# Kernel tuning notes

Hardware: AMD Instinct MI355X
Metric: run time of the kernel (lower is better)

## Reference

```python
import jax, jax.numpy as jnp
import numpy as np

N, F_IN, H, D = 4096, 512, 4, 64  # nodes, in_features, num_heads, head_dim (out_features = H*D = 256)
NEG_BIG = -9e15


def setup_inputs() -> dict:
    key = jax.random.key(0)
    k_x, k_adj, k_W, k_a = jax.random.split(key, 4)
    x = jax.random.normal(k_x, (N, F_IN), dtype=jnp.float32)
    adj = jax.random.randint(k_adj, (N, N), 0, 2, dtype=jnp.int32)
    # xavier_uniform-like scales
    W = jax.random.normal(k_W, (H, F_IN, D), dtype=jnp.float32) * np.float32((6.0 / (F_IN + D)) ** 0.5)
    a = jax.random.normal(k_a, (H, 2 * D), dtype=jnp.float32) * np.float32(0.1)
    bias = jnp.zeros((H * D,), dtype=jnp.float32)
    return {"x": x, "adj": adj, "W": W, "a": a, "bias": bias}


def reference(x, adj, W, a, bias):
    # Wx per head: [H, N, D]
    Wx = jnp.einsum('nf,hfd->hnd', x, W)
    # e[h,i,j] = leaky_relu(a[h,:D].Wx[h,i] + a[h,D:].Wx[h,j]) -- same math as concat form
    s_src = jnp.einsum('hnd,hd->hn', Wx, a[:, :D])  # [H, N]
    s_dst = jnp.einsum('hnd,hd->hn', Wx, a[:, D:])  # [H, N]
    e = jax.nn.leaky_relu(s_src[:, :, None] + s_dst[:, None, :], negative_slope=0.2)  # [H, N, N]
    masked = jnp.where(adj[None, :, :] > 0, e, jnp.float32(NEG_BIG))
    att = jax.nn.softmax(masked, axis=-1)  # row-wise softmax, [H, N, N]
    h = jnp.einsum('hij,hjd->hid', att, Wx)  # [H, N, D]
    out = h.transpose(1, 0, 2).reshape(x.shape[0], -1) + bias  # [N, H*D]
    return jax.nn.relu(out)
```

## Files before the change

### kernel.cpp

```cpp
#include <hip/hip_runtime.h>
#include <hip/hip_bf16.h>

#define NN   4096
#define FIN  512
#define NH   4
#define DD   64

typedef float f32x4 __attribute__((ext_vector_type(4)));
typedef short s16x8 __attribute__((ext_vector_type(8)));

__device__ __forceinline__ void gld_lds16(const void* g, void* l) {
  __builtin_amdgcn_global_load_lds(
      (const __attribute__((address_space(1))) void*)g,
      (__attribute__((address_space(3))) void*)l, 16, 0, 0);
}

__device__ __forceinline__ short bfbits(float f) {
  union { float f; unsigned u; } v; v.f = f;
  unsigned r = v.u + 0x7FFFu + ((v.u >> 16) & 1u);
  return (short)(r >> 16);
}

__device__ __forceinline__ int pkbf(float a, float b) {
  union { float f; unsigned u; } va, vb;
  va.f = a; vb.f = b;
  unsigned ra = (va.u + 0x7FFFu + ((va.u >> 16) & 1u)) >> 16;
  unsigned rb = (vb.u + 0x7FFFu + ((vb.u >> 16) & 1u)) & 0xFFFF0000u;
  return (int)(ra | rb);
}

__device__ __forceinline__ float hexp2(float x) {
#if __has_builtin(__builtin_amdgcn_exp2f)
  return __builtin_amdgcn_exp2f(x);
#else
  return __builtin_exp2f(x);
#endif
}

__global__ __launch_bounds__(512) void gat_k1(
    const float* __restrict__ x, const float* __restrict__ W,
    const float* __restrict__ a,
    short* __restrict__ WxT, float* __restrict__ ssrc, float* __restrict__ sdst)
{
  __shared__ __align__(16) char sm[34816];
  short* As = (short*)sm;
  short* Bs = (short*)(sm + 17408);
  float* Cs = (float*)sm;

  const int bx = blockIdx.x;
  const int h  = bx >> 6;
  const int r  = bx & 63;
  const int n0 = r * 64;
  const int t  = threadIdx.x;
  const int w  = t >> 6, lane = t & 63;
  const int lm = lane & 15, q = lane >> 4;
  const int rs = w & 3, cs = w >> 2;

  f32x4 acc[2] = {};
  const float* Wh = W + (size_t)h * (FIN * DD);

  for (int kq = 0; kq < 4; ++kq) {
    {
      const int row = t >> 3, fl = (t & 7) * 16;
      const float* xp = x + (size_t)(n0 + row) * FIN + kq * 128 + fl;
      float4 v0 = ((const float4*)xp)[0];
      float4 v1 = ((const float4*)xp)[1];
      float4 v2 = ((const float4*)xp)[2];
      float4 v3 = ((const float4*)xp)[3];
      union { short s[8]; int4 v; } u0, u1;
      u0.s[0]=bfbits(v0.x); u0.s[1]=bfbits(v0.y); u0.s[2]=bfbits(v0.z); u0.s[3]=bfbits(v0.w);
      u0.s[4]=bfbits(v1.x); u0.s[5]=bfbits(v1.y); u0.s[6]=bfbits(v1.z); u0.s[7]=bfbits(v1.w);
      u1.s[0]=bfbits(v2.x); u1.s[1]=bfbits(v2.y); u1.s[2]=bfbits(v2.z); u1.s[3]=bfbits(v2.w);
      u1.s[4]=bfbits(v3.x); u1.s[5]=bfbits(v3.y); u1.s[6]=bfbits(v3.z); u1.s[7]=bfbits(v3.w);
      *(int4*)(As + row * 136 + fl)     = u0.v;
      *(int4*)(As + row * 136 + fl + 8) = u1.v;
    }
    {
      const int fl = t >> 2, dc = (t & 3) * 16;
      const float* wp = Wh + (size_t)(kq * 128 + fl) * DD + dc;
      float4 w0 = ((const float4*)wp)[0];
      float4 w1 = ((const float4*)wp)[1];
      float4 w2 = ((const float4*)wp)[2];
      float4 w3 = ((const float4*)wp)[3];
      Bs[(dc+ 0)*136+fl]=bfbits(w0.x); Bs[(dc+ 1)*136+fl]=bfbits(w0.y);
      Bs[(dc+ 2)*136+fl]=bfbits(w0.z); Bs[(dc+ 3)*136+fl]=bfbits(w0.w);
      Bs[(dc+ 4)*136+fl]=bfbits(w1.x); Bs[(dc+ 5)*136+fl]=bfbits(w1.y);
      Bs[(dc+ 6)*136+fl]=bfbits(w1.z); Bs[(dc+ 7)*136+fl]=bfbits(w1.w);
      Bs[(dc+ 8)*136+fl]=bfbits(w2.x); Bs[(dc+ 9)*136+fl]=bfbits(w2.y);
      Bs[(dc+10)*136+fl]=bfbits(w2.z); Bs[(dc+11)*136+fl]=bfbits(w2.w);
      Bs[(dc+12)*136+fl]=bfbits(w3.x); Bs[(dc+13)*136+fl]=bfbits(w3.y);
      Bs[(dc+14)*136+fl]=bfbits(w3.z); Bs[(dc+15)*136+fl]=bfbits(w3.w);
    }
    __syncthreads();
#pragma unroll
    for (int s = 0; s < 4; ++s) {
      s16x8 af = *(const s16x8*)(As + (rs * 16 + lm) * 136 + s * 32 + q * 8);
#pragma unroll
      for (int c = 0; c < 2; ++c) {
        s16x8 bf = *(const s16x8*)(Bs + (cs * 32 + c * 16 + lm) * 136 + s * 32 + q * 8);
        acc[c] = __builtin_amdgcn_mfma_f32_16x16x32_bf16(af, bf, acc[c], 0, 0, 0);
      }
    }
    __syncthreads();
  }

#pragma unroll
  for (int c = 0; c < 2; ++c)
#pragma unroll
    for (int g = 0; g < 4; ++g)
      Cs[(cs * 32 + c * 16 + lm) * 65 + (rs * 16 + q * 4 + g)] = acc[c][g];
  __syncthreads();

  {
    const int d = t >> 3, nc = (t & 7) * 8;
    union { short s[8]; int4 v; } u;
#pragma unroll
    for (int e = 0; e < 8; ++e) u.s[e] = bfbits(Cs[d * 65 + nc + e]);
    *(int4*)(WxT + (size_t)(h * 64 + d) * NN + n0 + nc) = u.v;
  }
  if (t < 128) {
    const int n = t & 63;
    const int isdst = t >> 6;
    const float* av = a + h * 128 + isdst * 64;
    float s = 0.f;
#pragma unroll 8
    for (int d = 0; d < 64; ++d) s = fmaf(Cs[d * 65 + n], av[d], s);
    const float LOG2E = 1.4426950408889634f;
    (isdst ? sdst : ssrc)[h * NN + n0 + n] = s * LOG2E;
  }
}

__global__ __launch_bounds__(512) void gat_k2(
    const int* __restrict__ adj, const short* __restrict__ WxT,
    const float* __restrict__ ssrc, const float* __restrict__ sdst,
    const float* __restrict__ bias, float* __restrict__ out)
{
  __shared__ __align__(16) char sm[65536];
  short* VT  = (short*)sm;
  float* MRG = (float*)sm;
  float* Lm  = (float*)(sm + 52224);

  const int bx = blockIdx.x;
  const int h  = bx >> 6;
  const int r  = bx & 63;
  const int t  = threadIdx.x;
  const int w  = t >> 6, lane = t & 63;
  const int ms = w >> 2, kc = w & 3;
  const int lm = lane & 15, q = lane >> 4;

  const int i0 = r * 64 + ms * 32 + lm;
  const int i1 = i0 + 16;
  const float src0 = ssrc[h * NN + i0] - 1000.0f;
  const float src1 = ssrc[h * NN + i1] - 1000.0f;

  const short one = 0x3F80;
  s16x8 bones = {};
  if (lm == 0) {
    bones[0]=one; bones[1]=one; bones[2]=one; bones[3]=one;
    bones[4]=one; bones[5]=one; bones[6]=one; bones[7]=one;
  }

  f32x4 acc[2][4] = {};
  f32x4 accl[2] = {};

  const short* gstage = WxT + (size_t)(h * 64 + (lane >> 2)) * NN
                        + w * 32 + (lane & 3) * 8;

  int4   pa[2][8];
  float4 ps[2][4];
  const int jq = kc * 64 + q * 8;

#define LOAD_REGS(set, jb2)                                                   \
  {                                                                           \
    _Pragma("unroll")                                                         \
    for (int s = 0; s < 2; ++s) {                                             \
      const int j = (jb2) * 256 + jq + s * 32;                                \
      const int4* a0 = (const int4*)(adj + (size_t)i0 * NN + j);              \
      const int4* a1 = (const int4*)(adj + (size_t)i1 * NN + j);              \
      pa[set][s*4+0] = a0[0]; pa[set][s*4+1] = a0[1];                         \
      pa[set][s*4+2] = a1[0]; pa[set][s*4+3] = a1[1];                         \
      const float4* sd = (const float4*)(sdst + h * NN + j);                  \
      ps[set][s*2+0] = sd[0]; ps[set][s*2+1] = sd[1];                         \
    }                                                                         \
  }

#pragma unroll
  for (int k = 0; k < 4; ++k)
    gld_lds16(gstage + (size_t)(k * 16) * NN, VT + w * 2048 + k * 512);
  LOAD_REGS(0, 0)
  __syncthreads();

#pragma unroll
  for (int jb = 0; jb < 16; ++jb) {
    const int cur = jb & 1, nxt = cur ^ 1;
    if (jb < 15) {
#pragma unroll
      for (int k = 0; k < 4; ++k)
        gld_lds16(gstage + (size_t)(k * 16) * NN + (jb + 1) * 256,
                  VT + nxt * 16384 + w * 2048 + k * 512);
      LOAD_REGS(nxt, jb + 1)
    }

    const short* Vc = VT + cur * 16384 + kc * 4096;
#pragma unroll
    for (int s = 0; s < 2; ++s) {
      s16x8 bf[4];
#pragma unroll
      for (int c = 0; c < 4; ++c)
        bf[c] = *(const s16x8*)(Vc + s * 2048 + (c * 16 + lm) * 32 + q * 8);
#pragma unroll
      for (int rf = 0; rf < 2; ++rf) {
        const float src_i = rf ? src1 : src0;
        const int4 A0 = pa[cur][s * 4 + rf * 2];
        const int4 A1 = pa[cur][s * 4 + rf * 2 + 1];
        const float4 S0 = ps[cur][s * 2];
        const float4 S1 = ps[cur][s * 2 + 1];
        float p[8];
#define PGEN(dv, av, idx)                                                     \
        { float tp = src_i + (dv);                                            \
          float u  = fmaxf(tp, fmaf(tp, 0.2f, -800.0f));                      \
          u = fmaf((float)(av), 1000.0f, u);                                  \
          p[idx] = hexp2(u); }
        PGEN(S0.x, A0.x, 0) PGEN(S0.y, A0.y, 1)
        PGEN(S0.z, A0.z, 2) PGEN(S0.w, A0.w, 3)
        PGEN(S1.x, A1.x, 4) PGEN(S1.y, A1.y, 5)
        PGEN(S1.z, A1.z, 6) PGEN(S1.w, A1.w, 7)
#undef PGEN
        union { int i4[4]; s16x8 v; } af;
        af.i4[0] = pkbf(p[0], p[1]);
        af.i4[1] = pkbf(p[2], p[3]);
        af.i4[2] = pkbf(p[4], p[5]);
        af.i4[3] = pkbf(p[6], p[7]);
#pragma unroll
        for (int c = 0; c < 4; ++c)
          acc[rf][c] = __builtin_amdgcn_mfma_f32_16x16x32_bf16(af.v, bf[c], acc[rf][c], 0, 0, 0);
        accl[rf] = __builtin_amdgcn_mfma_f32_16x16x32_bf16(af.v, bones, accl[rf], 0, 0, 0);
      }
    }
    __syncthreads();
  }
#undef LOAD_REGS

  if (lm == 0) {
#pragma unroll
    for (int rf = 0; rf < 2; ++rf)
#pragma unroll
      for (int g = 0; g < 4; ++g)
        Lm[kc * 64 + ms * 32 + rf * 16 + q * 4 + g] = accl[rf][g];
  }
  if (kc != 0) {
#pragma unroll
    for (int rf = 0; rf < 2; ++rf)
#pragma unroll
      for (int c = 0; c < 4; ++c)
#pragma unroll
        for (int g = 0; g < 4; ++g)
          MRG[((kc - 1) * 64 + ms * 32 + rf * 16 + q * 4 + g) * 68 + c * 16 + lm] = acc[rf][c][g];
  }
  __syncthreads();
  if (kc == 0) {
#pragma unroll
    for (int rf = 0; rf < 2; ++rf) {
#pragma unroll
      for (int g = 0; g < 4; ++g) {
        const int row = ms * 32 + rf * 16 + q * 4 + g;
        float l = Lm[row] + Lm[64 + row] + Lm[128 + row] + Lm[192 + row];
        const float inv = 1.0f / l;
        const int grow = r * 64 + row;
#pragma unroll
        for (int c = 0; c < 4; ++c) {
          const int col = c * 16 + lm;
          float v = acc[rf][c][g]
                  + MRG[(row) * 68 + col]
                  + MRG[(64 + row) * 68 + col]
                  + MRG[(128 + row) * 68 + col];
          float o = fmaf(v, inv, bias[h * 64 + col]);
          out[(size_t)grow * 256 + h * 64 + col] = fmaxf(o, 0.0f);
        }
      }
    }
  }
}

extern "C" void kernel_launch(void* const* d_in, const int* in_sizes, int n_in,
                              void* d_out, int out_size, void* d_ws, size_t ws_size,
                              hipStream_t stream) {
  const float* x    = (const float*)d_in[0];
  const int*   adj  = (const int*)d_in[1];
  const float* W    = (const float*)d_in[2];
  const float* a    = (const float*)d_in[3];
  const float* bias = (const float*)d_in[4];
  float* out = (float*)d_out;

  short* WxT  = (short*)d_ws;
  float* ssrc = (float*)((char*)d_ws + (size_t)NH * DD * NN * 2);
  float* sdst = ssrc + NH * NN;

  gat_k1<<<256, 512, 0, stream>>>(x, W, a, WxT, ssrc, sdst);
  gat_k2<<<256, 512, 0, stream>>>(adj, WxT, ssrc, sdst, bias, out);
}
```

Before: 156.0 us.

## Retile GAT kernels: split heads across waves, drop LDS staging of V

The first kernel now uses 32-row tiles with 256 threads and 512 blocks, doubling its block count. The attention kernel now processes 32 rows per block for a pair of heads, with each wave taking a 1024-column slice. Adjacency rows are shared through L2 between the two heads of a pair. The LDS double-buffered prefetch of V and the per-step barriers are removed, and V fragments and adj/sdst now load directly from global memory into registers. This cuts synchronisation and LDS traffic, at the risk of exposed global-load latency with no explicit prefetch pipelining.

```diff
diff --git a/kernel.cpp b/kernel.cpp
--- a/kernel.cpp
+++ b/kernel.cpp
@@ -8,12 +8,6 @@
 
 typedef float f32x4 __attribute__((ext_vector_type(4)));
 typedef short s16x8 __attribute__((ext_vector_type(8)));
-
-__device__ __forceinline__ void gld_lds16(const void* g, void* l) {
-  __builtin_amdgcn_global_load_lds(
-      (const __attribute__((address_space(1))) void*)g,
-      (__attribute__((address_space(3))) void*)l, 16, 0, 0);
-}
 
 __device__ __forceinline__ short bfbits(float f) {
   union { float f; unsigned u; } v; v.f = f;
@@ -37,67 +31,61 @@
 #endif
 }
 
-__global__ __launch_bounds__(512) void gat_k1(
+__global__ __launch_bounds__(256) void gat_k1(
     const float* __restrict__ x, const float* __restrict__ W,
     const float* __restrict__ a,
     short* __restrict__ WxT, float* __restrict__ ssrc, float* __restrict__ sdst)
 {
-  __shared__ __align__(16) char sm[34816];
-  short* As = (short*)sm;
-  short* Bs = (short*)(sm + 17408);
-  float* Cs = (float*)sm;
-
-  const int bx = blockIdx.x;
-  const int h  = bx >> 6;
-  const int r  = bx & 63;
-  const int n0 = r * 64;
+  __shared__ short As[32 * 72];
+  __shared__ short Bs[64 * 72];
+  __shared__ float Cs[64 * 33];
+
+  const int blk = blockIdx.x;
+  const int h  = blk & 3;
+  const int rr = blk >> 2;
+  const int n0 = rr * 32;
   const int t  = threadIdx.x;
   const int w  = t >> 6, lane = t & 63;
   const int lm = lane & 15, q = lane >> 4;
-  const int rs = w & 3, cs = w >> 2;
+  const int wr = w & 1, wc = w >> 1;
 
   f32x4 acc[2] = {};
   const float* Wh = W + (size_t)h * (FIN * DD);
 
-  for (int kq = 0; kq < 4; ++kq) {
+  for (int kq = 0; kq < 8; ++kq) {
     {
-      const int row = t >> 3, fl = (t & 7) * 16;
-      const float* xp = x + (size_t)(n0 + row) * FIN + kq * 128 + fl;
+      const int row = t >> 3, fc = (t & 7) * 8;
+      const float* xp = x + (size_t)(n0 + row) * FIN + kq * 64 + fc;
       float4 v0 = ((const float4*)xp)[0];
       float4 v1 = ((const float4*)xp)[1];
-      float4 v2 = ((const float4*)xp)[2];
-      float4 v3 = ((const float4*)xp)[3];
-      union { short s[8]; int4 v; } u0, u1;
-      u0.s[0]=bfbits(v0.x); u0.s[1]=bfbits(v0.y); u0.s[2]=bfbits(v0.z); u0.s[3]=bfbits(v0.w);
-      u0.s[4]=bfbits(v1.x); u0.s[5]=bfbits(v1.y); u0.s[6]=bfbits(v1.z); u0.s[7]=bfbits(v1.w);
-      u1.s[0]=bfbits(v2.x); u1.s[1]=bfbits(v2.y); u1.s[2]=bfbits(v2.z); u1.s[3]=bfbits(v2.w);
-      u1.s[4]=bfbits(v3.x); u1.s[5]=bfbits(v3.y); u1.s[6]=bfbits(v3.z); u1.s[7]=bfbits(v3.w);
-      *(int4*)(As + row * 136 + fl)     = u0.v;
-      *(int4*)(As + row * 136 + fl + 8) = u1.v;
+      union { short s[8]; int4 v; } u;
+      u.s[0]=bfbits(v0.x); u.s[1]=bfbits(v0.y); u.s[2]=bfbits(v0.z); u.s[3]=bfbits(v0.w);
+      u.s[4]=bfbits(v1.x); u.s[5]=bfbits(v1.y); u.s[6]=bfbits(v1.z); u.s[7]=bfbits(v1.w);
+      *(int4*)(As + row * 72 + fc) = u.v;
     }
     {
       const int fl = t >> 2, dc = (t & 3) * 16;
-      const float* wp = Wh + (size_t)(kq * 128 + fl) * DD + dc;
+      const float* wp = Wh + (size_t)(kq * 64 + fl) * DD + dc;
       float4 w0 = ((const float4*)wp)[0];
       float4 w1 = ((const float4*)wp)[1];
       float4 w2 = ((const float4*)wp)[2];
       float4 w3 = ((const float4*)wp)[3];
-      Bs[(dc+ 0)*136+fl]=bfbits(w0.x); Bs[(dc+ 1)*136+fl]=bfbits(w0.y);
-      Bs[(dc+ 2)*136+fl]=bfbits(w0.z); Bs[(dc+ 3)*136+fl]=bfbits(w0.w);
-      Bs[(dc+ 4)*136+fl]=bfbits(w1.x); Bs[(dc+ 5)*136+fl]=bfbits(w1.y);
-      Bs[(dc+ 6)*136+fl]=bfbits(w1.z); Bs[(dc+ 7)*136+fl]=bfbits(w1.w);
-      Bs[(dc+ 8)*136+fl]=bfbits(w2.x); Bs[(dc+ 9)*136+fl]=bfbits(w2.y);
-      Bs[(dc+10)*136+fl]=bfbits(w2.z); Bs[(dc+11)*136+fl]=bfbits(w2.w);
-      Bs[(dc+12)*136+fl]=bfbits(w3.x); Bs[(dc+13)*136+fl]=bfbits(w3.y);
-      Bs[(dc+14)*136+fl]=bfbits(w3.z); Bs[(dc+15)*136+fl]=bfbits(w3.w);
+      Bs[(dc+ 0)*72+fl]=bfbits(w0.x); Bs[(dc+ 1)*72+fl]=bfbits(w0.y);
+      Bs[(dc+ 2)*72+fl]=bfbits(w0.z); Bs[(dc+ 3)*72+fl]=bfbits(w0.w);
+      Bs[(dc+ 4)*72+fl]=bfbits(w1.x); Bs[(dc+ 5)*72+fl]=bfbits(w1.y);
+      Bs[(dc+ 6)*72+fl]=bfbits(w1.z); Bs[(dc+ 7)*72+fl]=bfbits(w1.w);
+      Bs[(dc+ 8)*72+fl]=bfbits(w2.x); Bs[(dc+ 9)*72+fl]=bfbits(w2.y);
+      Bs[(dc+10)*72+fl]=bfbits(w2.z); Bs[(dc+11)*72+fl]=bfbits(w2.w);
+      Bs[(dc+12)*72+fl]=bfbits(w3.x); Bs[(dc+13)*72+fl]=bfbits(w3.y);
+      Bs[(dc+14)*72+fl]=bfbits(w3.z); Bs[(dc+15)*72+fl]=bfbits(w3.w);
     }
     __syncthreads();
 #pragma unroll
-    for (int s = 0; s < 4; ++s) {
-      s16x8 af = *(const s16x8*)(As + (rs * 16 + lm) * 136 + s * 32 + q * 8);
+    for (int s = 0; s < 2; ++s) {
+      s16x8 af = *(const s16x8*)(As + (wr * 16 + lm) * 72 + s * 32 + q * 8);
 #pragma unroll
       for (int c = 0; c < 2; ++c) {
-        s16x8 bf = *(const s16x8*)(Bs + (cs * 32 + c * 16 + lm) * 136 + s * 32 + q * 8);
+        s16x8 bf = *(const s16x8*)(Bs + (wc * 32 + c * 16 + lm) * 72 + s * 32 + q * 8);
         acc[c] = __builtin_amdgcn_mfma_f32_16x16x32_bf16(af, bf, acc[c], 0, 0, 0);
       }
     }
@@ -108,48 +96,49 @@
   for (int c = 0; c < 2; ++c)
 #pragma unroll
     for (int g = 0; g < 4; ++g)
-      Cs[(cs * 32 + c * 16 + lm) * 65 + (rs * 16 + q * 4 + g)] = acc[c][g];
+      Cs[(wc * 32 + c * 16 + lm) * 33 + (wr * 16 + q * 4 + g)] = acc[c][g];
   __syncthreads();
 
   {
-    const int d = t >> 3, nc = (t & 7) * 8;
+    const int d = t >> 2, nc = (t & 3) * 8;
     union { short s[8]; int4 v; } u;
 #pragma unroll
-    for (int e = 0; e < 8; ++e) u.s[e] = bfbits(Cs[d * 65 + nc + e]);
+    for (int e = 0; e < 8; ++e) u.s[e] = bfbits(Cs[d * 33 + nc + e]);
     *(int4*)(WxT + (size_t)(h * 64 + d) * NN + n0 + nc) = u.v;
   }
-  if (t < 128) {
-    const int n = t & 63;
-    const int isdst = t >> 6;
+  if (t < 64) {
+    const int n = t & 31;
+    const int isdst = t >> 5;
     const float* av = a + h * 128 + isdst * 64;
     float s = 0.f;
 #pragma unroll 8
-    for (int d = 0; d < 64; ++d) s = fmaf(Cs[d * 65 + n], av[d], s);
+    for (int d = 0; d < 64; ++d) s = fmaf(Cs[d * 33 + n], av[d], s);
     const float LOG2E = 1.4426950408889634f;
     (isdst ? sdst : ssrc)[h * NN + n0 + n] = s * LOG2E;
   }
 }
 
-__global__ __launch_bounds__(512) void gat_k2(
+__global__ __launch_bounds__(512, 2) void gat_k2(
     const int* __restrict__ adj, const short* __restrict__ WxT,
     const float* __restrict__ ssrc, const float* __restrict__ sdst,
     const float* __restrict__ bias, float* __restrict__ out)
 {
-  __shared__ __align__(16) char sm[65536];
-  short* VT  = (short*)sm;
-  float* MRG = (float*)sm;
-  float* Lm  = (float*)(sm + 52224);
-
-  const int bx = blockIdx.x;
-  const int h  = bx >> 6;
-  const int r  = bx & 63;
-  const int t  = threadIdx.x;
-  const int w  = t >> 6, lane = t & 63;
-  const int ms = w >> 2, kc = w & 3;
+  __shared__ float MRG[6][32][68];
+  __shared__ float Lm[2][4][32];
+
+  const int blk = blockIdx.x;
+  const int rr    = ((blk >> 4) << 3) | (blk & 7);
+  const int hpair = (blk >> 3) & 1;
+  const int t = threadIdx.x;
+  const int w = t >> 6, lane = t & 63;
   const int lm = lane & 15, q = lane >> 4;
-
-  const int i0 = r * 64 + ms * 32 + lm;
-  const int i1 = i0 + 16;
+  const int hp = w & 1;
+  const int h  = hpair * 2 + hp;
+  const int jc = w >> 1;
+  const int jbase = jc * 1024;
+  const int ib = rr * 32;
+  const int i0 = ib + lm, i1 = i0 + 16;
+
   const float src0 = ssrc[h * NN + i0] - 1000.0f;
   const float src1 = ssrc[h * NN + i1] - 1000.0f;
 
@@ -163,117 +152,88 @@
   f32x4 acc[2][4] = {};
   f32x4 accl[2] = {};
 
-  const short* gstage = WxT + (size_t)(h * 64 + (lane >> 2)) * NN
-                        + w * 32 + (lane & 3) * 8;
-
-  int4   pa[2][8];
-  float4 ps[2][4];
-  const int jq = kc * 64 + q * 8;
-
-#define LOAD_REGS(set, jb2)                                                   \
-  {                                                                           \
-    _Pragma("unroll")                                                         \
-    for (int s = 0; s < 2; ++s) {                                             \
-      const int j = (jb2) * 256 + jq + s * 32;                                \
-      const int4* a0 = (const int4*)(adj + (size_t)i0 * NN + j);              \
-      const int4* a1 = (const int4*)(adj + (size_t)i1 * NN + j);              \
-      pa[set][s*4+0] = a0[0]; pa[set][s*4+1] = a0[1];                         \
-      pa[set][s*4+2] = a1[0]; pa[set][s*4+3] = a1[1];                         \
-      const float4* sd = (const float4*)(sdst + h * NN + j);                  \
-      ps[set][s*2+0] = sd[0]; ps[set][s*2+1] = sd[1];                         \
-    }                                                                         \
-  }
-
-#pragma unroll
-  for (int k = 0; k < 4; ++k)
-    gld_lds16(gstage + (size_t)(k * 16) * NN, VT + w * 2048 + k * 512);
-  LOAD_REGS(0, 0)
+  const short* Vb    = WxT + (size_t)(h * 64) * NN;
+  const int*   arow0 = adj + (size_t)i0 * NN;
+  const int*   arow1 = adj + (size_t)i1 * NN;
+  const float* sdh   = sdst + h * NN;
+
+#pragma unroll 2
+  for (int js = 0; js < 32; ++js) {
+    const int j0 = jbase + js * 32 + q * 8;
+
+    s16x8 bf[4];
+#pragma unroll
+    for (int c = 0; c < 4; ++c)
+      bf[c] = *(const s16x8*)(Vb + (size_t)(c * 16 + lm) * NN + j0);
+
+    const int4* A0p = (const int4*)(arow0 + j0);
+    const int4* A1p = (const int4*)(arow1 + j0);
+    int4 A00 = A0p[0], A01 = A0p[1];
+    int4 A10 = A1p[0], A11 = A1p[1];
+    const float4* Sp = (const float4*)(sdh + j0);
+    float4 S0 = Sp[0], S1 = Sp[1];
+
+#pragma unroll
+    for (int rf = 0; rf < 2; ++rf) {
+      const float src_i = rf ? src1 : src0;
+      const int4 Aa = rf ? A10 : A00;
+      const int4 Ab = rf ? A11 : A01;
+      float p[8];
+#define PGEN(dv, av, idx)                                                     \
+      { float tp = src_i + (dv);                                              \
+        float u  = fmaxf(tp, fmaf(tp, 0.2f, -800.0f));                        \
+        u = fmaf((float)(av), 1000.0f, u);                                    \
+        p[idx] = hexp2(u); }
+      PGEN(S0.x, Aa.x, 0) PGEN(S0.y, Aa.y, 1)
+      PGEN(S0.z, Aa.z, 2) PGEN(S0.w, Aa.w, 3)
+      PGEN(S1.x, Ab.x, 4) PGEN(S1.y, Ab.y, 5)
+      PGEN(S1.z, Ab.z, 6) PGEN(S1.w, Ab.w, 7)
+#undef PGEN
+      union { int i4[4]; s16x8 v; } af;
+      af.i4[0] = pkbf(p[0], p[1]);
+      af.i4[1] = pkbf(p[2], p[3]);
+      af.i4[2] = pkbf(p[4], p[5]);
+      af.i4[3] = pkbf(p[6], p[7]);
+#pragma unroll
+      for (int c = 0; c < 4; ++c)
+        acc[rf][c] = __builtin_amdgcn_mfma_f32_16x16x32_bf16(af.v, bf[c], acc[rf][c], 0, 0, 0);
+      accl[rf] = __builtin_amdgcn_mfma_f32_16x16x32_bf16(af.v, bones, accl[rf], 0, 0, 0);
+    }
+  }
+
+  if (jc != 0) {
+#pragma unroll
+    for (int rf = 0; rf < 2; ++rf)
+#pragma unroll
+      for (int c = 0; c < 4; ++c)
+#pragma unroll
+        for (int g = 0; g < 4; ++g)
+          MRG[hp * 3 + jc - 1][rf * 16 + q * 4 + g][c * 16 + lm] = acc[rf][c][g];
+  }
+  if (lm == 0) {
+#pragma unroll
+    for (int rf = 0; rf < 2; ++rf)
+#pragma unroll
+      for (int g = 0; g < 4; ++g)
+        Lm[hp][jc][rf * 16 + q * 4 + g] = accl[rf][g];
+  }
   __syncthreads();
-
-#pragma unroll
-  for (int jb = 0; jb < 16; ++jb) {
-    const int cur = jb & 1, nxt = cur ^ 1;
-    if (jb < 15) {
-#pragma unroll
-      for (int k = 0; k < 4; ++k)
-        gld_lds16(gstage + (size_t)(k * 16) * NN + (jb + 1) * 256,
-                  VT + nxt * 16384 + w * 2048 + k * 512);
-      LOAD_REGS(nxt, jb + 1)
-    }
-
-    const short* Vc = VT + cur * 16384 + kc * 4096;
-#pragma unroll
-    for (int s = 0; s < 2; ++s) {
-      s16x8 bf[4];
-#pragma unroll
-      for (int c = 0; c < 4; ++c)
-        bf[c] = *(const s16x8*)(Vc + s * 2048 + (c * 16 + lm) * 32 + q * 8);
-#pragma unroll
-      for (int rf = 0; rf < 2; ++rf) {
-        const float src_i = rf ? src1 : src0;
-        const int4 A0 = pa[cur][s * 4 + rf * 2];
-        const int4 A1 = pa[cur][s * 4 + rf * 2 + 1];
-        const float4 S0 = ps[cur][s * 2];
-        const float4 S1 = ps[cur][s * 2 + 1];
-        float p[8];
-#define PGEN(dv, av, idx)                                                     \
-        { float tp = src_i + (dv);                                            \
-          float u  = fmaxf(tp, fmaf(tp, 0.2f, -800.0f));                      \
-          u = fmaf((float)(av), 1000.0f, u);                                  \
-          p[idx] = hexp2(u); }
-        PGEN(S0.x, A0.x, 0) PGEN(S0.y, A0.y, 1)
-        PGEN(S0.z, A0.z, 2) PGEN(S0.w, A0.w, 3)
-        PGEN(S1.x, A1.x, 4) PGEN(S1.y, A1.y, 5)
-        PGEN(S1.z, A1.z, 6) PGEN(S1.w, A1.w, 7)
-#undef PGEN
-        union { int i4[4]; s16x8 v; } af;
-        af.i4[0] = pkbf(p[0], p[1]);
-        af.i4[1] = pkbf(p[2], p[3]);
-        af.i4[2] = pkbf(p[4], p[5]);
-        af.i4[3] = pkbf(p[6], p[7]);
-#pragma unroll
-        for (int c = 0; c < 4; ++c)
-          acc[rf][c] = __builtin_amdgcn_mfma_f32_16x16x32_bf16(af.v, bf[c], acc[rf][c], 0, 0, 0);
-        accl[rf] = __builtin_amdgcn_mfma_f32_16x16x32_bf16(af.v, bones, accl[rf], 0, 0, 0);
-      }
-    }
-    __syncthreads();
-  }
-#undef LOAD_REGS
-
-  if (lm == 0) {
-#pragma unroll
-    for (int rf = 0; rf < 2; ++rf)
-#pragma unroll
-      for (int g = 0; g < 4; ++g)
-        Lm[kc * 64 + ms * 32 + rf * 16 + q * 4 + g] = accl[rf][g];
-  }
-  if (kc != 0) {
-#pragma unroll
-    for (int rf = 0; rf < 2; ++rf)
-#pragma unroll
-      for (int c = 0; c < 4; ++c)
-#pragma unroll
-        for (int g = 0; g < 4; ++g)
-          MRG[((kc - 1) * 64 + ms * 32 + rf * 16 + q * 4 + g) * 68 + c * 16 + lm] = acc[rf][c][g];
-  }
-  __syncthreads();
-  if (kc == 0) {
+  if (jc == 0) {
 #pragma unroll
     for (int rf = 0; rf < 2; ++rf) {
 #pragma unroll
       for (int g = 0; g < 4; ++g) {
-        const int row = ms * 32 + rf * 16 + q * 4 + g;
-        float l = Lm[row] + Lm[64 + row] + Lm[128 + row] + Lm[192 + row];
+        const int row = rf * 16 + q * 4 + g;
+        const float l = Lm[hp][0][row] + Lm[hp][1][row] + Lm[hp][2][row] + Lm[hp][3][row];
         const float inv = 1.0f / l;
-        const int grow = r * 64 + row;
+        const int grow = ib + row;
 #pragma unroll
         for (int c = 0; c < 4; ++c) {
           const int col = c * 16 + lm;
           float v = acc[rf][c][g]
-                  + MRG[(row) * 68 + col]
-                  + MRG[(64 + row) * 68 + col]
-                  + MRG[(128 + row) * 68 + col];
+                  + MRG[hp * 3 + 0][row][col]
+                  + MRG[hp * 3 + 1][row][col]
+                  + MRG[hp * 3 + 2][row][col];
           float o = fmaf(v, inv, bias[h * 64 + col]);
           out[(size_t)grow * 256 + h * 64 + col] = fmaxf(o, 0.0f);
         }
@@ -296,6 +256,6 @@
   float* ssrc = (float*)((char*)d_ws + (size_t)NH * DD * NN * 2);
   float* sdst = ssrc + NH * NN;
 
-  gat_k1<<<256, 512, 0, stream>>>(x, W, a, WxT, ssrc, sdst);
+  gat_k1<<<512, 256, 0, stream>>>(x, W, a, WxT, ssrc, sdst);
   gat_k2<<<256, 512, 0, stream>>>(adj, WxT, ssrc, sdst, bias, out);
 }
```

New measurement: 182.0 us. 1.17x slower.
